# Kernel optimization log

Hardware: AMD Instinct MI355X
Metric: run time of the kernel (lower is better)

The kernel has to match this reference:

```python
import jax, jax.numpy as jnp
import numpy as np

TOP_K = 2  # MoE top-k routing


def setup_inputs() -> dict:
    key = jax.random.key(0)
    ks = jax.random.split(key, 5)
    B, D, H, O, N = 8192, 3072, 128, 10, 8
    scale_g = 1.0 / np.sqrt(D)
    return {
        "x": jax.random.normal(ks[0], (B, D), dtype=jnp.float32),
        "Wg": jax.random.normal(ks[1], (D, N), dtype=jnp.float32) * scale_g,
        "bg": jnp.zeros((N,), dtype=jnp.float32),
        "W1": jax.random.normal(ks[2], (N, D, H), dtype=jnp.float32) * scale_g,
        "b1": jnp.zeros((N, H), dtype=jnp.float32),
        "W2": jax.random.normal(ks[3], (N, H, O), dtype=jnp.float32) * (1.0 / np.sqrt(H)),
        "b2": jnp.zeros((N, O), dtype=jnp.float32),
    }


def reference(x, Wg, bg, W1, b1, W2, b2):
    # Gating: logits -> top-k -> softmax over the k selected logits
    g = x @ Wg + bg                                  # [B, N]
    tv, ti = jax.lax.top_k(g, TOP_K)                 # [B, k]
    w = jax.nn.softmax(tv, axis=-1)                  # [B, k]
    # Expert MLPs, computed densely over all experts (vectorized dispatch)
    h = jax.nn.relu(jnp.einsum('bd,edh->beh', x, W1) + b1)   # [B, N, H]
    y = jnp.einsum('beh,eho->beo', h, W2) + b2               # [B, N, O]
    # Combine: gather each token's k selected expert outputs, weight, sum
    ysel = jnp.take_along_axis(y, ti[:, :, None], axis=1)    # [B, k, O]
    return jnp.sum(w[:, :, None] * ysel, axis=1)             # [B, O]
```

## Files before the change

kernel.cpp:

```cpp
#include <hip/hip_runtime.h>
#include <hip/hip_bf16.h>

#define B_TOK 8192
#define D_DIM 3072
#define H_DIM 128
#define O_DIM 10
#define N_EXP 8

#define BM 128
#define BK 64
#define HLDS_STRIDE 136

typedef __bf16 bf16x8 __attribute__((ext_vector_type(8)));
typedef float  f32x4  __attribute__((ext_vector_type(4)));

__device__ __forceinline__ unsigned short f2bf(float f) {
  unsigned int u = __float_as_uint(f);
  unsigned int r = (u + 0x7FFFu + ((u >> 16) & 1u)) >> 16;
  return (unsigned short)r;
}

__device__ __forceinline__ void async16(const void* g, void* l) {
  __builtin_amdgcn_global_load_lds(
      (const __attribute__((address_space(1))) void*)g,
      (__attribute__((address_space(3))) void*)l,
      16, 0, 0);
}

__global__ void k0_w1_transpose(const float* __restrict__ W1,
                                unsigned short* __restrict__ w1t) {
  __shared__ unsigned short tile[32][33];
  const int e  = blockIdx.z;
  const int d0 = blockIdx.x * 32;
  const int h0 = blockIdx.y * 32;
  const int tx = threadIdx.x;
  const int ty = threadIdx.y;
  const float* src = W1 + ((size_t)e * D_DIM + d0) * H_DIM + h0;
#pragma unroll
  for (int k = 0; k < 4; ++k) {
    int r = ty + 8 * k;
    tile[r][tx] = f2bf(src[(size_t)r * H_DIM + tx]);
  }
  __syncthreads();
  unsigned short* dst = w1t + ((size_t)e * H_DIM + h0) * D_DIM + d0;
#pragma unroll
  for (int k = 0; k < 4; ++k) {
    int r = ty + 8 * k;
    dst[(size_t)r * D_DIM + tx] = tile[tx][r];
  }
}

__global__ __launch_bounds__(256) void k1_gate_convert(
    const float* __restrict__ x, const float* __restrict__ Wg,
    const float* __restrict__ bg, unsigned short* __restrict__ xb,
    float4* __restrict__ route) {
  __shared__ float wg_lds[N_EXP * D_DIM];
  const int tid = threadIdx.x;

  for (int f = tid; f < D_DIM * N_EXP / 4; f += 256) {
    const float4 v = ((const float4*)Wg)[f];
    const int d  = f >> 1;
    const int nh = (f & 1) * 4;
    wg_lds[(nh + 0) * D_DIM + d] = v.x;
    wg_lds[(nh + 1) * D_DIM + d] = v.y;
    wg_lds[(nh + 2) * D_DIM + d] = v.z;
    wg_lds[(nh + 3) * D_DIM + d] = v.w;
  }
  __syncthreads();

  const int lane = tid & 63;
  const int wv   = tid >> 6;

  for (int ti = 0; ti < 8; ++ti) {
    const int tk = blockIdx.x * 32 + ti * 4 + wv;
    const float* xr = x + (size_t)tk * D_DIM;
    unsigned short* xbr = xb + (size_t)tk * D_DIM;

    float acc[N_EXP];
#pragma unroll
    for (int n = 0; n < N_EXP; ++n) acc[n] = 0.f;

#pragma unroll 12
    for (int jj = 0; jj < D_DIM / 64; ++jj) {
      const int d = jj * 64 + lane;
      const float xs = xr[d];
      xbr[d] = f2bf(xs);
#pragma unroll
      for (int n = 0; n < N_EXP; ++n)
        acc[n] = fmaf(xs, wg_lds[n * D_DIM + d], acc[n]);
    }

#pragma unroll
    for (int n = 0; n < N_EXP; ++n) {
#pragma unroll
      for (int off = 32; off > 0; off >>= 1)
        acc[n] += __shfl_xor(acc[n], off, 64);
    }
    if (lane == 0) {
      float g[N_EXP];
#pragma unroll
      for (int n = 0; n < N_EXP; ++n) g[n] = acc[n] + bg[n];
      int i0 = 0;
#pragma unroll
      for (int n = 1; n < N_EXP; ++n) if (g[n] > g[i0]) i0 = n;
      int i1 = (i0 == 0) ? 1 : 0;
#pragma unroll
      for (int n = 0; n < N_EXP; ++n) if (n != i0 && g[n] > g[i1]) i1 = n;
      float e1 = expf(g[i1] - g[i0]);
      float inv = 1.f / (1.f + e1);
      route[tk] = make_float4(inv, e1 * inv, __int_as_float(i0), __int_as_float(i1));
    }
  }
}

__global__ __launch_bounds__(256) void k2_experts(
    const unsigned short* __restrict__ xb,
    const unsigned short* __restrict__ w1t,
    const float* __restrict__ b1,
    const float* __restrict__ W2,
    const float* __restrict__ b2,
    float* __restrict__ yall) {
  __shared__ __align__(16) unsigned short sm[(34816 + 4096) / 2];
  unsigned short* a_lds   = sm;
  unsigned short* b_lds   = sm + 128 * 64;
  unsigned short* h_lds   = sm;
  unsigned short* w2t_lds = sm + 128 * HLDS_STRIDE;

  const int mblk = blockIdx.x;
  const int e    = blockIdx.y;
  const int tid  = threadIdx.x;
  const int lane = tid & 63;
  const int wv   = tid >> 6;

  const float* W2e = W2 + (size_t)e * H_DIM * O_DIM;
  for (int idx = tid; idx < 16 * 128; idx += 256) {
    int o = idx >> 7, hh = idx & 127;
    float v = (o < O_DIM) ? W2e[hh * O_DIM + o] : 0.f;
    w2t_lds[idx] = f2bf(v);
  }

  const int mhalf = (wv >> 1) * 64;
  const int nhalf = (wv & 1) * 64;

  f32x4 acc[4][4];
#pragma unroll
  for (int i = 0; i < 4; ++i)
#pragma unroll
    for (int j = 0; j < 4; ++j)
      acc[i][j] = (f32x4){0.f, 0.f, 0.f, 0.f};

  const unsigned short* A_base  = xb + (size_t)(mblk * BM) * D_DIM;
  const unsigned short* Bt_base = w1t + (size_t)e * H_DIM * D_DIM;

  const int srow = wv * 32 + (lane >> 3);
  const int scol = (lane & 7) * 8;

  for (int k0 = 0; k0 < D_DIM; k0 += BK) {
#pragma unroll
    for (int j = 0; j < 4; ++j) {
      const int r = srow + j * 8;
      async16(A_base  + (size_t)r * D_DIM + k0 + scol, a_lds + (wv * 32 + j * 8) * BK);
      async16(Bt_base + (size_t)r * D_DIM + k0 + scol, b_lds + (wv * 32 + j * 8) * BK);
    }
    __syncthreads();
#pragma unroll
    for (int kk = 0; kk < 2; ++kk) {
      bf16x8 af[4], bfr[4];
      const int krd = kk * 32 + (lane >> 4) * 8;
#pragma unroll
      for (int mi = 0; mi < 4; ++mi)
        af[mi] = *(const bf16x8*)(a_lds + (mhalf + mi * 16 + (lane & 15)) * BK + krd);
#pragma unroll
      for (int ni = 0; ni < 4; ++ni)
        bfr[ni] = *(const bf16x8*)(b_lds + (nhalf + ni * 16 + (lane & 15)) * BK + krd);
#pragma unroll
      for (int mi = 0; mi < 4; ++mi)
#pragma unroll
        for (int ni = 0; ni < 4; ++ni)
          acc[mi][ni] = __builtin_amdgcn_mfma_f32_16x16x32_bf16(af[mi], bfr[ni], acc[mi][ni], 0, 0, 0);
    }
    __syncthreads();
  }

  const float* b1e = b1 + e * H_DIM;
#pragma unroll
  for (int ni = 0; ni < 4; ++ni) {
    const int col  = nhalf + ni * 16 + (lane & 15);
    const float bias = b1e[col];
#pragma unroll
    for (int mi = 0; mi < 4; ++mi) {
      const int rbase = mhalf + mi * 16 + ((lane >> 4) << 2);
#pragma unroll
      for (int r = 0; r < 4; ++r) {
        float v = acc[mi][ni][r] + bias;
        v = v > 0.f ? v : 0.f;
        h_lds[(rbase + r) * HLDS_STRIDE + col] = f2bf(v);
      }
    }
  }
  __syncthreads();

  f32x4 acc2[2];
  acc2[0] = (f32x4){0.f, 0.f, 0.f, 0.f};
  acc2[1] = (f32x4){0.f, 0.f, 0.f, 0.f};
#pragma unroll
  for (int ks = 0; ks < 4; ++ks) {
    const int krd = ks * 32 + (lane >> 4) * 8;
    bf16x8 bfr = *(const bf16x8*)(w2t_lds + (lane & 15) * 128 + krd);
#pragma unroll
    for (int mi = 0; mi < 2; ++mi) {
      bf16x8 afr = *(const bf16x8*)(h_lds + (wv * 32 + mi * 16 + (lane & 15)) * HLDS_STRIDE + krd);
      acc2[mi] = __builtin_amdgcn_mfma_f32_16x16x32_bf16(afr, bfr, acc2[mi], 0, 0, 0);
    }
  }
  const int o = lane & 15;
  if (o < O_DIM) {
    const float bias2 = b2[e * O_DIM + o];
#pragma unroll
    for (int mi = 0; mi < 2; ++mi) {
#pragma unroll
      for (int r = 0; r < 4; ++r) {
        const int row = mblk * BM + wv * 32 + mi * 16 + ((lane >> 4) << 2) + r;
        yall[((size_t)row * N_EXP + e) * O_DIM + o] = acc2[mi][r] + bias2;
      }
    }
  }
}

__global__ __launch_bounds__(256) void k3_combine(
    const float* __restrict__ yall, const float4* __restrict__ route,
    float* __restrict__ out) {
  const int g = blockIdx.x * 256 + threadIdx.x;
  if (g >= B_TOK * O_DIM) return;
  const int b = g / O_DIM, o = g - b * O_DIM;
  const float4 r = route[b];
  const int i0 = __float_as_int(r.z), i1 = __float_as_int(r.w);
  out[g] = r.x * yall[((size_t)b * N_EXP + i0) * O_DIM + o] +
           r.y * yall[((size_t)b * N_EXP + i1) * O_DIM + o];
}

extern "C" void kernel_launch(void* const* d_in, const int* in_sizes, int n_in,
                              void* d_out, int out_size, void* d_ws, size_t ws_size,
                              hipStream_t stream) {
  const float* x  = (const float*)d_in[0];
  const float* Wg = (const float*)d_in[1];
  const float* bg = (const float*)d_in[2];
  const float* W1 = (const float*)d_in[3];
  const float* b1 = (const float*)d_in[4];
  const float* W2 = (const float*)d_in[5];
  const float* b2 = (const float*)d_in[6];
  float* out = (float*)d_out;

  char* ws = (char*)d_ws;
  unsigned short* xb  = (unsigned short*)ws;
  unsigned short* w1t = (unsigned short*)(ws + 50331648);
  float4* route       = (float4*)(ws + 56623104);
  float* yall         = (float*)(ws + 56754176);

  k0_w1_transpose<<<dim3(96, 4, 8), dim3(32, 8), 0, stream>>>(W1, w1t);
  k1_gate_convert<<<dim3(B_TOK / 32), dim3(256), 0, stream>>>(x, Wg, bg, xb, route);
  k2_experts<<<dim3(B_TOK / BM, N_EXP), dim3(256), 0, stream>>>(xb, w1t, b1, W2, b2, yall);
  k3_combine<<<dim3((B_TOK * O_DIM + 255) / 256), dim3(256), 0, stream>>>(yall, route, out);
}
```

Baseline: 263.6 us.

## Route tokens sparsely to selected experts instead of computing all experts densely

The gating kernel now counts tokens per expert with atomics and records each token's slot, and a new single-block kernel builds a per-expert token list. The expert GEMM kernel gathers only the routed token rows, so roughly a quarter of the dense FLOPs remain, and blocks past each expert's count exit early. The gate kernel also uses 512 threads and processes four tokens per wave so each Wg value loaded from LDS is reused across four tokens. The costs are an extra serial scatter kernel, a memset, gathered (less regular) A-row loads, and load imbalance across experts.

```diff
diff --git a/kernel.cpp b/kernel.cpp
--- a/kernel.cpp
+++ b/kernel.cpp
@@ -50,14 +50,16 @@
   }
 }
 
-__global__ __launch_bounds__(256) void k1_gate_convert(
+__global__ __launch_bounds__(512) void k1_gate_convert(
     const float* __restrict__ x, const float* __restrict__ Wg,
     const float* __restrict__ bg, unsigned short* __restrict__ xb,
-    float4* __restrict__ route) {
+    int4* __restrict__ idx4, float2* __restrict__ wts, int* __restrict__ cnt) {
   __shared__ float wg_lds[N_EXP * D_DIM];
+  __shared__ int lcnt[N_EXP], gbase[N_EXP];
   const int tid = threadIdx.x;
 
-  for (int f = tid; f < D_DIM * N_EXP / 4; f += 256) {
+  if (tid < N_EXP) lcnt[tid] = 0;
+  for (int f = tid; f < D_DIM * N_EXP / 4; f += 512) {
     const float4 v = ((const float4*)Wg)[f];
     const int d  = f >> 1;
     const int nh = (f & 1) * 4;
@@ -70,36 +72,57 @@
 
   const int lane = tid & 63;
   const int wv   = tid >> 6;
-
-  for (int ti = 0; ti < 8; ++ti) {
-    const int tk = blockIdx.x * 32 + ti * 4 + wv;
-    const float* xr = x + (size_t)tk * D_DIM;
-    unsigned short* xbr = xb + (size_t)tk * D_DIM;
-
-    float acc[N_EXP];
-#pragma unroll
-    for (int n = 0; n < N_EXP; ++n) acc[n] = 0.f;
-
-#pragma unroll 12
-    for (int jj = 0; jj < D_DIM / 64; ++jj) {
-      const int d = jj * 64 + lane;
-      const float xs = xr[d];
-      xbr[d] = f2bf(xs);
-#pragma unroll
-      for (int n = 0; n < N_EXP; ++n)
-        acc[n] = fmaf(xs, wg_lds[n * D_DIM + d], acc[n]);
-    }
-
+  const int tk0  = blockIdx.x * 32 + wv * 4;
+
+  const float* xr0 = x + (size_t)(tk0 + 0) * D_DIM;
+  const float* xr1 = x + (size_t)(tk0 + 1) * D_DIM;
+  const float* xr2 = x + (size_t)(tk0 + 2) * D_DIM;
+  const float* xr3 = x + (size_t)(tk0 + 3) * D_DIM;
+  unsigned short* xw0 = xb + (size_t)(tk0 + 0) * D_DIM;
+  unsigned short* xw1 = xb + (size_t)(tk0 + 1) * D_DIM;
+  unsigned short* xw2 = xb + (size_t)(tk0 + 2) * D_DIM;
+  unsigned short* xw3 = xb + (size_t)(tk0 + 3) * D_DIM;
+
+  float acc[4][N_EXP];
+#pragma unroll
+  for (int t = 0; t < 4; ++t)
+#pragma unroll
+    for (int n = 0; n < N_EXP; ++n) acc[t][n] = 0.f;
+
+#pragma unroll 2
+  for (int jj = 0; jj < D_DIM / 64; ++jj) {
+    const int d = jj * 64 + lane;
+    float w8[N_EXP];
+#pragma unroll
+    for (int n = 0; n < N_EXP; ++n) w8[n] = wg_lds[n * D_DIM + d];
+    const float x0 = xr0[d], x1 = xr1[d], x2 = xr2[d], x3 = xr3[d];
+    xw0[d] = f2bf(x0); xw1[d] = f2bf(x1); xw2[d] = f2bf(x2); xw3[d] = f2bf(x3);
 #pragma unroll
     for (int n = 0; n < N_EXP; ++n) {
+      acc[0][n] = fmaf(x0, w8[n], acc[0][n]);
+      acc[1][n] = fmaf(x1, w8[n], acc[1][n]);
+      acc[2][n] = fmaf(x2, w8[n], acc[2][n]);
+      acc[3][n] = fmaf(x3, w8[n], acc[3][n]);
+    }
+  }
+
+#pragma unroll
+  for (int t = 0; t < 4; ++t)
+#pragma unroll
+    for (int n = 0; n < N_EXP; ++n) {
 #pragma unroll
       for (int off = 32; off > 0; off >>= 1)
-        acc[n] += __shfl_xor(acc[n], off, 64);
-    }
-    if (lane == 0) {
+        acc[t][n] += __shfl_xor(acc[t][n], off, 64);
+    }
+
+  int li0[4], li1[4], lp0[4], lp1[4];
+  float lw0[4], lw1[4];
+  if (lane == 0) {
+#pragma unroll
+    for (int t = 0; t < 4; ++t) {
       float g[N_EXP];
 #pragma unroll
-      for (int n = 0; n < N_EXP; ++n) g[n] = acc[n] + bg[n];
+      for (int n = 0; n < N_EXP; ++n) g[n] = acc[t][n] + bg[n];
       int i0 = 0;
 #pragma unroll
       for (int n = 1; n < N_EXP; ++n) if (g[n] > g[i0]) i0 = n;
@@ -108,8 +131,42 @@
       for (int n = 0; n < N_EXP; ++n) if (n != i0 && g[n] > g[i1]) i1 = n;
       float e1 = expf(g[i1] - g[i0]);
       float inv = 1.f / (1.f + e1);
-      route[tk] = make_float4(inv, e1 * inv, __int_as_float(i0), __int_as_float(i1));
-    }
+      li0[t] = i0; li1[t] = i1;
+      lw0[t] = inv; lw1[t] = e1 * inv;
+      lp0[t] = atomicAdd(&lcnt[i0], 1);
+      lp1[t] = atomicAdd(&lcnt[i1], 1);
+    }
+  }
+  __syncthreads();
+  if (tid < N_EXP) gbase[tid] = atomicAdd(&cnt[tid], lcnt[tid]);
+  __syncthreads();
+  if (lane == 0) {
+#pragma unroll
+    for (int t = 0; t < 4; ++t) {
+      idx4[tk0 + t] = make_int4(li0[t], gbase[li0[t]] + lp0[t],
+                                li1[t], gbase[li1[t]] + lp1[t]);
+      wts[tk0 + t]  = make_float2(lw0[t], lw1[t]);
+    }
+  }
+}
+
+__global__ __launch_bounds__(256) void k1b_scan_scatter(
+    const int* __restrict__ cnt, int* __restrict__ off_g,
+    const int4* __restrict__ idx4, int* __restrict__ tlist) {
+  __shared__ int off[N_EXP + 1];
+  if (threadIdx.x == 0) {
+    int s = 0;
+#pragma unroll
+    for (int n = 0; n < N_EXP; ++n) { off[n] = s; s += cnt[n]; }
+    off[N_EXP] = s;
+#pragma unroll
+    for (int n = 0; n <= N_EXP; ++n) off_g[n] = off[n];
+  }
+  __syncthreads();
+  for (int t = threadIdx.x; t < B_TOK; t += 256) {
+    const int4 r = idx4[t];
+    tlist[off[r.x] + r.y] = t;
+    tlist[off[r.z] + r.w] = t;
   }
 }
 
@@ -119,15 +176,21 @@
     const float* __restrict__ b1,
     const float* __restrict__ W2,
     const float* __restrict__ b2,
-    float* __restrict__ yall) {
+    const int* __restrict__ cnt, const int* __restrict__ off_g,
+    const int* __restrict__ tlist,
+    float* __restrict__ ypair) {
+  const int e    = blockIdx.y;
+  const int n_e  = cnt[e];
+  const int row0 = blockIdx.x * BM;
+  if (row0 >= n_e) return;
+  const int off_e = off_g[e];
+
   __shared__ __align__(16) unsigned short sm[(34816 + 4096) / 2];
   unsigned short* a_lds   = sm;
   unsigned short* b_lds   = sm + 128 * 64;
   unsigned short* h_lds   = sm;
   unsigned short* w2t_lds = sm + 128 * HLDS_STRIDE;
 
-  const int mblk = blockIdx.x;
-  const int e    = blockIdx.y;
   const int tid  = threadIdx.x;
   const int lane = tid & 63;
   const int wv   = tid >> 6;
@@ -149,18 +212,24 @@
     for (int j = 0; j < 4; ++j)
       acc[i][j] = (f32x4){0.f, 0.f, 0.f, 0.f};
 
-  const unsigned short* A_base  = xb + (size_t)(mblk * BM) * D_DIM;
-  const unsigned short* Bt_base = w1t + (size_t)e * H_DIM * D_DIM;
-
   const int srow = wv * 32 + (lane >> 3);
   const int scol = (lane & 7) * 8;
 
+  const unsigned short* Arow[4];
+#pragma unroll
+  for (int j = 0; j < 4; ++j) {
+    int gr = row0 + srow + j * 8;
+    gr = gr < n_e ? gr : n_e - 1;
+    Arow[j] = xb + (size_t)tlist[off_e + gr] * D_DIM + scol;
+  }
+  const unsigned short* Bt_base = w1t + (size_t)e * H_DIM * D_DIM + scol;
+
   for (int k0 = 0; k0 < D_DIM; k0 += BK) {
 #pragma unroll
     for (int j = 0; j < 4; ++j) {
       const int r = srow + j * 8;
-      async16(A_base  + (size_t)r * D_DIM + k0 + scol, a_lds + (wv * 32 + j * 8) * BK);
-      async16(Bt_base + (size_t)r * D_DIM + k0 + scol, b_lds + (wv * 32 + j * 8) * BK);
+      async16(Arow[j] + k0, a_lds + (wv * 32 + j * 8) * BK);
+      async16(Bt_base + (size_t)r * D_DIM + k0, b_lds + (wv * 32 + j * 8) * BK);
     }
     __syncthreads();
 #pragma unroll
@@ -220,23 +289,25 @@
     for (int mi = 0; mi < 2; ++mi) {
 #pragma unroll
       for (int r = 0; r < 4; ++r) {
-        const int row = mblk * BM + wv * 32 + mi * 16 + ((lane >> 4) << 2) + r;
-        yall[((size_t)row * N_EXP + e) * O_DIM + o] = acc2[mi][r] + bias2;
+        const int rl = wv * 32 + mi * 16 + ((lane >> 4) << 2) + r;
+        if (row0 + rl < n_e)
+          ypair[(size_t)(off_e + row0 + rl) * 16 + o] = acc2[mi][r] + bias2;
       }
     }
   }
 }
 
 __global__ __launch_bounds__(256) void k3_combine(
-    const float* __restrict__ yall, const float4* __restrict__ route,
+    const float* __restrict__ ypair, const int4* __restrict__ idx4,
+    const float2* __restrict__ wts, const int* __restrict__ off_g,
     float* __restrict__ out) {
   const int g = blockIdx.x * 256 + threadIdx.x;
   if (g >= B_TOK * O_DIM) return;
   const int b = g / O_DIM, o = g - b * O_DIM;
-  const float4 r = route[b];
-  const int i0 = __float_as_int(r.z), i1 = __float_as_int(r.w);
-  out[g] = r.x * yall[((size_t)b * N_EXP + i0) * O_DIM + o] +
-           r.y * yall[((size_t)b * N_EXP + i1) * O_DIM + o];
+  const int4 r = idx4[b];
+  const float2 w = wts[b];
+  out[g] = w.x * ypair[(size_t)(off_g[r.x] + r.y) * 16 + o] +
+           w.y * ypair[(size_t)(off_g[r.z] + r.w) * 16 + o];
 }
 
 extern "C" void kernel_launch(void* const* d_in, const int* in_sizes, int n_in,
@@ -254,11 +325,19 @@
   char* ws = (char*)d_ws;
   unsigned short* xb  = (unsigned short*)ws;
   unsigned short* w1t = (unsigned short*)(ws + 50331648);
-  float4* route       = (float4*)(ws + 56623104);
-  float* yall         = (float*)(ws + 56754176);
+  int4*   idx4  = (int4*)  (ws + 56623104);
+  float2* wts   = (float2*)(ws + 56754176);
+  int*    cnt   = (int*)   (ws + 56819712);
+  int*    off_g = (int*)   (ws + 56819744);
+  int*    tlist = (int*)   (ws + 56819840);
+  float*  ypair = (float*) (ws + 56885376);
 
   k0_w1_transpose<<<dim3(96, 4, 8), dim3(32, 8), 0, stream>>>(W1, w1t);
-  k1_gate_convert<<<dim3(B_TOK / 32), dim3(256), 0, stream>>>(x, Wg, bg, xb, route);
-  k2_experts<<<dim3(B_TOK / BM, N_EXP), dim3(256), 0, stream>>>(xb, w1t, b1, W2, b2, yall);
-  k3_combine<<<dim3((B_TOK * O_DIM + 255) / 256), dim3(256), 0, stream>>>(yall, route, out);
-}
+  hipMemsetAsync(cnt, 0, N_EXP * sizeof(int), stream);
+  k1_gate_convert<<<dim3(B_TOK / 32), dim3(512), 0, stream>>>(x, Wg, bg, xb, idx4, wts, cnt);
+  k1b_scan_scatter<<<dim3(1), dim3(256), 0, stream>>>(cnt, off_g, idx4, tlist);
+  k2_experts<<<dim3(B_TOK / BM, N_EXP), dim3(256), 0, stream>>>(
+      xb, w1t, b1, W2, b2, cnt, off_g, tlist, ypair);
+  k3_combine<<<dim3((B_TOK * O_DIM + 255) / 256), dim3(256), 0, stream>>>(
+      ypair, idx4, wts, off_g, out);
+}
```

Result: slower. 283.5 us (+7.5%).
